# Kernel optimization log

Hardware: AMD Instinct MI355X
Metric: run time of the kernel (lower is better)

The kernel has to match this reference:

```python
import jax, jax.numpy as jnp
import numpy as np

E = 1024      # embed_dim
QH = 16       # query heads
KVH = 4       # kv heads
HD = E // QH  # head_dim = 64
KVE = HD * KVH  # 256
EPS = 1e-5
ROPE_BASE = 10000.0


def rope(x, d):
    # Faithful to the source RoPE: d == number of heads (x.shape[-2]),
    # and the 'sequence' axis of the cache is x.shape[0] (the batch dim).
    # rope(x) = x*cos + (x*sin) * neg_half(x)  (note: nonlinear in x).
    b = x.shape[0]
    theta = 1.0 / (ROPE_BASE ** (jnp.arange(0, d, 2, dtype=jnp.float32) / d))  # (d//2,)
    seq_idx = jnp.arange(b, dtype=jnp.float32)                                 # (b,)
    idx_theta = seq_idx[:, None] * theta[None, :]                              # (b, d//2)
    idx2 = jnp.concatenate([idx_theta, idx_theta], axis=-1)                    # (b, d)
    # cached shape (b,1,1,d); source permutes (0,1,3,2) -> (b,1,d,1)
    cos = jnp.cos(idx2)[:, None, :, None]  # (b,1,d,1)
    sin = jnp.sin(idx2)[:, None, :, None]
    d2 = d // 2
    # split of the LAST dim (head_dim) at d//2 == num_heads//2, as in source
    neg = jnp.concatenate([-x[..., d2:], x[..., :d2]], axis=-1)
    return x * cos + (x * sin) * neg


def setup_inputs() -> dict:
    key = jax.random.key(0)
    ks = jax.random.split(key, 12)
    b, n = 1, 2048

    def xavier(k, shape):
        fan_out, fan_in = shape
        std = (2.0 / (fan_in + fan_out)) ** 0.5
        return jax.random.normal(k, shape, dtype=jnp.float32) * std

    return {
        "query": jax.random.normal(ks[0], (b, n, E), dtype=jnp.float32),
        "key": jax.random.normal(ks[1], (b, n, E), dtype=jnp.float32),
        "value": jax.random.normal(ks[2], (b, n, E), dtype=jnp.float32),
        "Wq": xavier(ks[3], (E, E)),
        "bq": jnp.zeros((E,), jnp.float32),
        "Wk": xavier(ks[4], (KVE, E)),
        "bk": jnp.zeros((KVE,), jnp.float32),
        "Wv": xavier(ks[5], (KVE, E)),
        "bv": jnp.zeros((KVE,), jnp.float32),
        "gamma": jnp.ones((E,), jnp.float32),
        "beta": jnp.zeros((E,), jnp.float32),
    }


def reference(query, key, value, Wq, bq, Wk, bk, Wv, bv, gamma, beta):
    b, n, _ = query.shape
    q = query @ Wq.T + bq            # (b,n,E)
    k = key @ Wk.T + bk              # (b,n,KVE)
    v = value @ Wv.T + bv            # (b,n,KVE)

    q = q.reshape(b, n, QH, HD)      # b n h d
    k = k.reshape(b, n, KVH, HD)
    v = v.reshape(b, n, KVH, HD)

    q = rope(q, QH)
    k = rope(k, KVH)

    # b n h d -> b h n d
    q = jnp.transpose(q, (0, 2, 1, 3))
    k = jnp.transpose(k, (0, 2, 1, 3))
    v = jnp.transpose(v, (0, 2, 1, 3))

    scale = float(HD) ** 0.5
    q = q / scale

    g = QH // KVH
    # 'b (h g) n d -> b g h n d' : h outer, g inner
    q = q.reshape(b, KVH, g, n, HD)              # (b, h, g, n, d)
    q = jnp.transpose(q, (0, 2, 1, 3, 4))        # (b, g, h, n, d)

    sim = jnp.einsum('bghnd,bhsd->bghns', q, k)  # (b,g,h,n,s)
    attn = jax.nn.softmax(sim, axis=-1)
    out = jnp.einsum('bghns,bhsd->bghnd', attn, v)

    # 'b g h n d -> b n (h g) d'
    out = jnp.transpose(out, (0, 3, 2, 1, 4))    # (b, n, h, g, d)
    x = out.reshape(b, n, QH * HD)               # (b, n, E)

    # LayerNorm (biased variance, as in torch)
    mu = jnp.mean(x, axis=-1, keepdims=True)
    var = jnp.mean((x - mu) ** 2, axis=-1, keepdims=True)
    x = (x - mu) * jax.lax.rsqrt(var + EPS) * gamma + beta

    # NOTE: source computes out_proj(x) but returns x, so out_proj is dead code.
    return x
```

## Files before the change

kernel.cpp:

```cpp
#include <hip/hip_runtime.h>
#include <math.h>

#define EDIM   1024
#define KVEDIM 256
#define HDIM   64
#define QHEADS 16

typedef __attribute__((ext_vector_type(8))) short short8;
typedef __attribute__((ext_vector_type(4))) float f32x4;

__device__ __forceinline__ unsigned pack2(float a, float b) {
    unsigned ua = __builtin_bit_cast(unsigned, a);
    unsigned ub = __builtin_bit_cast(unsigned, b);
    ua += 0x7fffu + ((ua >> 16) & 1u);
    ub += 0x7fffu + ((ub >> 16) & 1u);
    return (ua >> 16) | (ub & 0xffff0000u);
}
__device__ __forceinline__ short f2b(float a) {
    unsigned ua = __builtin_bit_cast(unsigned, a);
    ua += 0x7fffu + ((ua >> 16) & 1u);
    return (short)(ua >> 16);
}
__device__ __forceinline__ unsigned cvtpk(float a, float b) {
    unsigned r;
    asm("v_cvt_pk_bf16_f32 %0, %1, %2" : "=v"(r) : "v"(a), "v"(b));
    return r;
}

__global__ __launch_bounds__(256)
void cvt_bf16(const float* __restrict__ s0, const float* __restrict__ s1,
              const float* __restrict__ s2, const float* __restrict__ s3,
              const float* __restrict__ s4, const float* __restrict__ s5,
              short* __restrict__ d0, short* __restrict__ d1,
              short* __restrict__ d2, short* __restrict__ d3,
              short* __restrict__ d4, short* __restrict__ d5,
              int n0, int n1, int n2, int n3, int n4, int n5)
{
    const float* s; short* d; int n;
    switch (blockIdx.y) {
        case 0: s = s0; d = d0; n = n0; break;
        case 1: s = s1; d = d1; n = n1; break;
        case 2: s = s2; d = d2; n = n2; break;
        case 3: s = s3; d = d3; n = n3; break;
        case 4: s = s4; d = d4; n = n4; break;
        default: s = s5; d = d5; n = n5; break;
    }
    int i = ((int)blockIdx.x * 256 + threadIdx.x) * 8;
    if (i >= n) return;
    float4 a = *(const float4*)&s[i];
    float4 b = *(const float4*)&s[i + 4];
    uint4 o;
    o.x = pack2(a.x, a.y); o.y = pack2(a.z, a.w);
    o.z = pack2(b.x, b.y); o.w = pack2(b.z, b.w);
    *(uint4*)&d[i] = o;
}

__global__ __launch_bounds__(256)
void proj_gemm(const short* __restrict__ Aq, const short* __restrict__ Ak,
               const short* __restrict__ Av,
               const short* __restrict__ Wqb, const short* __restrict__ Wkb,
               const short* __restrict__ Wvb,
               const float* __restrict__ bq, const float* __restrict__ bk,
               const float* __restrict__ bv,
               short* __restrict__ Cq, short* __restrict__ Ck,
               short* __restrict__ Cv, float qscale)
{
    const int bid = blockIdx.x;
    const short* A; const short* W; const float* bias; short* C;
    int N, bm, bn; float scale;
    if (bid < 128) {
        A = Aq; W = Wqb; bias = bq; C = Cq; N = EDIM; scale = qscale;
        bm = (bid >> 3) * 128; bn = (bid & 7) * 128;
    } else if (bid < 160) {
        int i = bid - 128;
        A = Ak; W = Wkb; bias = bk; C = Ck; N = KVEDIM; scale = 1.0f;
        bm = (i >> 1) * 128; bn = (i & 1) * 128;
    } else {
        int i = bid - 160;
        A = Av; W = Wvb; bias = bv; C = Cv; N = KVEDIM; scale = 1.0f;
        bm = (i >> 1) * 128; bn = (i & 1) * 128;
    }
    const int K = EDIM;

    __shared__ short As[128 * 72];
    __shared__ short Ws[128 * 72];

    const int t = threadIdx.x, lane = t & 63, wv = t >> 6;
    const int lm = lane & 15, quad = lane >> 4;
    const int q8 = quad * 8, q4 = quad * 4;
    const int wm = (wv & 1) * 64, wn = (wv >> 1) * 64;
    const int sr = t >> 3, sc = (t & 7) * 8;

    f32x4 zero = {0.f, 0.f, 0.f, 0.f};
    f32x4 acc[4][4];
    #pragma unroll
    for (int i = 0; i < 4; ++i)
        #pragma unroll
        for (int j = 0; j < 4; ++j) acc[i][j] = zero;

    for (int k0 = 0; k0 < K; k0 += 64) {
        __syncthreads();
        #pragma unroll
        for (int i = 0; i < 4; ++i) {
            int r = sr + i * 32;
            *(uint4*)&As[r * 72 + sc] = *(const uint4*)&A[(size_t)(bm + r) * K + k0 + sc];
            *(uint4*)&Ws[r * 72 + sc] = *(const uint4*)&W[(size_t)(bn + r) * K + k0 + sc];
        }
        __syncthreads();
        #pragma unroll
        for (int ks = 0; ks < 2; ++ks) {
            short8 af[4], bfr[4];
            #pragma unroll
            for (int i = 0; i < 4; ++i)
                af[i] = *(const short8*)&As[(wm + i * 16 + lm) * 72 + ks * 32 + q8];
            #pragma unroll
            for (int j = 0; j < 4; ++j)
                bfr[j] = *(const short8*)&Ws[(wn + j * 16 + lm) * 72 + ks * 32 + q8];
            #pragma unroll
            for (int i = 0; i < 4; ++i)
                #pragma unroll
                for (int j = 0; j < 4; ++j)
                    acc[i][j] = __builtin_amdgcn_mfma_f32_16x16x32_bf16(
                        af[i], bfr[j], acc[i][j], 0, 0, 0);
        }
    }

    #pragma unroll
    for (int j = 0; j < 4; ++j) {
        float bj = bias[bn + wn + j * 16 + lm];
        #pragma unroll
        for (int i = 0; i < 4; ++i)
            #pragma unroll
            for (int r = 0; r < 4; ++r)
                C[(size_t)(bm + wm + i * 16 + q4 + r) * N + bn + wn + j * 16 + lm] =
                    f2b((acc[i][j][r] + bj) * scale);
    }
}

__global__ __launch_bounds__(256, 4)
void attn_mfma(const short* __restrict__ q, const short* __restrict__ k,
               const short* __restrict__ v, float* __restrict__ x,
               float* __restrict__ opart, float* __restrict__ lpart,
               int n, int s_len, int partial)
{
    __shared__ short Ks[64 * 64];
    __shared__ short Vs[4096];

    const int kvh = blockIdx.y;
    const int r0  = blockIdx.x * 16;
    const int t = threadIdx.x, lane = t & 63, wv = t >> 6;
    const int qh = (kvh << 2) | wv;
    const int lm = lane & 15, quad = lane >> 4, q8 = quad * 8;

    short8 qf0, qf1;
    {
        const short* qp = &q[(size_t)(r0 + lm) * EDIM + qh * HDIM];
        qf0 = *(const short8*)&qp[q8];
        qf1 = *(const short8*)&qp[32 + q8];
    }

    const f32x4 zero = {0.f, 0.f, 0.f, 0.f};
    f32x4 oacc[4] = {zero, zero, zero, zero};
    float lp = 0.f;

    const int sr  = t >> 2;
    const int scs = (t & 3) * 16;
    const int kw0 = sr * 64 + (scs ^ ((sr & 7) << 3));
    const int kw1 = sr * 64 + ((scs + 8) ^ ((sr & 7) << 3));
    const int vs4 = (t & 15) * 4;
    const int vd0 = (t >> 4) * 4;
    const int vktp = vs4 >> 5, vqd = (vs4 >> 2) & 3, vhf = (vs4 >> 4) & 1;

    const int krx  = q8 ^ ((lm & 7) << 3);
    const int krx2 = (32 + q8) ^ ((lm & 7) << 3);

    const int s_lo = (int)blockIdx.z * s_len;
    const int s_hi = s_lo + s_len;
    const size_t kbase = (size_t)kvh * HDIM;

    uint4 kra, krb;
    uint2 vrr[4];
    {
        const uint4* ks = (const uint4*)&k[(size_t)(s_lo + sr) * KVEDIM + kbase + scs];
        kra = ks[0]; krb = ks[1];
        #pragma unroll
        for (int i = 0; i < 4; ++i)
            vrr[i] = *(const uint2*)&v[(size_t)(s_lo + vs4 + i) * KVEDIM + kbase + vd0];
    }

    for (int s0 = s_lo; s0 < s_hi; s0 += 64) {
        *(uint4*)&Ks[kw0] = kra;
        *(uint4*)&Ks[kw1] = krb;
        #pragma unroll
        for (int j = 0; j < 4; ++j) {
            const unsigned sel = (j & 1) ? 0x07060302u : 0x05040100u;
            unsigned a0 = (j < 2) ? vrr[0].x : vrr[0].y;
            unsigned a1 = (j < 2) ? vrr[1].x : vrr[1].y;
            unsigned a2 = (j < 2) ? vrr[2].x : vrr[2].y;
            unsigned a3 = (j < 2) ? vrr[3].x : vrr[3].y;
            uint2 o;
            o.x = __builtin_amdgcn_perm(a1, a0, sel);
            o.y = __builtin_amdgcn_perm(a3, a2, sel);
            const int dd = vd0 + j;
            int slot = ((dd >> 4) << 7) + (vktp << 6) + (vqd << 4) + (dd & 15);
            slot ^= (slot >> 4) & 7;
            *(uint2*)&Vs[slot * 8 + vhf * 4] = o;
        }
        __syncthreads();

        if (s0 + 64 < s_hi) {
            const uint4* ks = (const uint4*)&k[(size_t)(s0 + 64 + sr) * KVEDIM + kbase + scs];
            kra = ks[0]; krb = ks[1];
            #pragma unroll
            for (int i = 0; i < 4; ++i)
                vrr[i] = *(const uint2*)&v[(size_t)(s0 + 64 + vs4 + i) * KVEDIM + kbase + vd0];
        }

        uint2 pa[4];
        #pragma unroll
        for (int kt = 0; kt < 4; ++kt) {
            const int krow = (kt * 16 + lm) * 64;
            short8 kf0 = *(const short8*)&Ks[krow + krx];
            short8 kf1 = *(const short8*)&Ks[krow + krx2];
            f32x4 s = zero;
            s = __builtin_amdgcn_mfma_f32_16x16x32_bf16(kf0, qf0, s, 0, 0, 0);
            s = __builtin_amdgcn_mfma_f32_16x16x32_bf16(kf1, qf1, s, 0, 0, 0);
            float p0 = exp2f(s[0]), p1 = exp2f(s[1]);
            float p2 = exp2f(s[2]), p3 = exp2f(s[3]);
            lp += (p0 + p1) + (p2 + p3);
            pa[kt].x = cvtpk(p0, p1);
            pa[kt].y = cvtpk(p2, p3);
        }

        uint4 ap0; ap0.x = pa[0].x; ap0.y = pa[0].y; ap0.z = pa[1].x; ap0.w = pa[1].y;
        uint4 ap1; ap1.x = pa[2].x; ap1.y = pa[2].y; ap1.z = pa[3].x; ap1.w = pa[3].y;
        #pragma unroll
        for (int dt = 0; dt < 4; ++dt) {
            int sb  = (dt << 7) + (quad << 4) + lm;
            int sx0 = sb ^ ((sb >> 4) & 7);
            int sb1 = sb + 64;
            int sx1 = sb1 ^ ((sb1 >> 4) & 7);
            oacc[dt] = __builtin_amdgcn_mfma_f32_16x16x32_bf16(
                __builtin_bit_cast(short8, ap0),
                *(const short8*)&Vs[sx0 * 8], oacc[dt], 0, 0, 0);
            oacc[dt] = __builtin_amdgcn_mfma_f32_16x16x32_bf16(
                __builtin_bit_cast(short8, ap1),
                *(const short8*)&Vs[sx1 * 8], oacc[dt], 0, 0, 0);
        }
        __syncthreads();
    }

    float lt = lp;
    lt += __shfl_xor(lt, 16);
    lt += __shfl_xor(lt, 32);

    if (partial) {
        float* xp = opart + (size_t)blockIdx.z * n * EDIM;
        if (lane < 16)
            lpart[(size_t)blockIdx.z * n * QHEADS + (size_t)(r0 + lane) * QHEADS + qh] = lt;
        #pragma unroll
        for (int r = 0; r < 4; ++r) {
            const int row = r0 + quad * 4 + r;
            #pragma unroll
            for (int dt = 0; dt < 4; ++dt)
                xp[(size_t)row * EDIM + qh * HDIM + dt * 16 + lm] = oacc[dt][r];
        }
    } else {
        float linv[4];
        #pragma unroll
        for (int r = 0; r < 4; ++r)
            linv[r] = 1.0f / __shfl(lt, quad * 4 + r);
        #pragma unroll
        for (int r = 0; r < 4; ++r) {
            const int row = r0 + quad * 4 + r;
            #pragma unroll
            for (int dt = 0; dt < 4; ++dt)
                x[(size_t)row * EDIM + qh * HDIM + dt * 16 + lm] = oacc[dt][r] * linv[r];
        }
    }
}

__global__ __launch_bounds__(256)
void ln_kernel(float* __restrict__ x, const float* __restrict__ gamma,
               const float* __restrict__ beta,
               const float* __restrict__ opart, const float* __restrict__ lpart,
               int nsplit, int n)
{
    const int row = blockIdx.x;
    const int t = threadIdx.x;

    float4 xv;
    if (nsplit > 0) {
        const int head = t >> 4;
        float l = 0.f;
        float4 s = {0.f, 0.f, 0.f, 0.f};
        for (int z = 0; z < nsplit; ++z) {
            const float4 o = *(const float4*)&opart[(size_t)z * n * EDIM +
                                                    (size_t)row * EDIM + t * 4];
            s.x += o.x; s.y += o.y; s.z += o.z; s.w += o.w;
            l += lpart[(size_t)z * n * QHEADS + (size_t)row * QHEADS + head];
        }
        const float inv = 1.f / l;
        xv.x = s.x * inv; xv.y = s.y * inv; xv.z = s.z * inv; xv.w = s.w * inv;
    } else {
        xv = *(const float4*)&x[(size_t)row * EDIM + t * 4];
    }

    float sm  = xv.x + xv.y + xv.z + xv.w;
    float sq = xv.x * xv.x + xv.y * xv.y + xv.z * xv.z + xv.w * xv.w;
    #pragma unroll
    for (int m = 1; m < 64; m <<= 1) {
        sm += __shfl_xor(sm, m);
        sq += __shfl_xor(sq, m);
    }
    __shared__ float ws_[4], wq_[4];
    const int wave = t >> 6;
    if ((t & 63) == 0) { ws_[wave] = sm; wq_[wave] = sq; }
    __syncthreads();
    sm = ws_[0] + ws_[1] + ws_[2] + ws_[3];
    sq = wq_[0] + wq_[1] + wq_[2] + wq_[3];

    const float mu   = sm * (1.f / EDIM);
    const float var  = sq * (1.f / EDIM) - mu * mu;
    const float rstd = rsqrtf(var + 1e-5f);

    float4 g = *(const float4*)&gamma[t * 4];
    float4 b = *(const float4*)&beta[t * 4];
    float4 o;
    o.x = (xv.x - mu) * rstd * g.x + b.x;
    o.y = (xv.y - mu) * rstd * g.y + b.y;
    o.z = (xv.z - mu) * rstd * g.z + b.z;
    o.w = (xv.w - mu) * rstd * g.w + b.w;
    *(float4*)&x[(size_t)row * EDIM + t * 4] = o;
}

extern "C" void kernel_launch(void* const* d_in, const int* in_sizes, int n_in,
                              void* d_out, int out_size, void* d_ws, size_t ws_size,
                              hipStream_t stream)
{
    const float* query = (const float*)d_in[0];
    const float* key   = (const float*)d_in[1];
    const float* value = (const float*)d_in[2];
    const float* Wq    = (const float*)d_in[3];
    const float* bq    = (const float*)d_in[4];
    const float* Wk    = (const float*)d_in[5];
    const float* bk    = (const float*)d_in[6];
    const float* Wv    = (const float*)d_in[7];
    const float* bv    = (const float*)d_in[8];
    const float* gamma = (const float*)d_in[9];
    const float* beta  = (const float*)d_in[10];
    float* out = (float*)d_out;

    const int n = in_sizes[0] / EDIM;

    short* qa  = (short*)d_ws;
    short* ka  = qa  + (size_t)n * EDIM;
    short* va  = ka  + (size_t)n * EDIM;
    short* wqb = va  + (size_t)n * EDIM;
    short* wkb = wqb + (size_t)EDIM * EDIM;
    short* wvb = wkb + (size_t)KVEDIM * EDIM;
    short* qb  = wvb + (size_t)KVEDIM * EDIM;
    short* kb  = qb  + (size_t)n * EDIM;
    short* vb  = kb  + (size_t)n * KVEDIM;
    short* ws_end = vb + (size_t)n * KVEDIM;

    const size_t base_bytes = (size_t)((char*)ws_end - (char*)d_ws);
    int nsplit = 0;
    {
        const int cand = 2;
        size_t need = base_bytes +
                      (size_t)cand * ((size_t)n * EDIM + (size_t)n * QHEADS) * sizeof(float);
        if ((n % (64 * cand)) == 0 && need <= ws_size) nsplit = cand;
    }
    float* opart = (float*)ws_end;
    float* lpart = opart + (size_t)(nsplit > 0 ? nsplit : 1) * n * EDIM;

    const float qscale = 0.125f * 1.44269504088896f;

    cvt_bf16<<<dim3(1024, 6), 256, 0, stream>>>(
        query, key, value, Wq, Wk, Wv,
        qa, ka, va, wqb, wkb, wvb,
        n * EDIM, n * EDIM, n * EDIM, EDIM * EDIM, KVEDIM * EDIM, KVEDIM * EDIM);

    proj_gemm<<<dim3(192), 256, 0, stream>>>(
        qa, ka, va, wqb, wkb, wvb, bq, bk, bv, qb, kb, vb, qscale);

    const int zdim  = (nsplit > 0) ? nsplit : 1;
    const int s_len = n / zdim;
    attn_mfma<<<dim3(n / 16, 4, zdim), 256, 0, stream>>>(
        qb, kb, vb, out, opart, lpart, n, s_len, nsplit > 0 ? 1 : 0);

    ln_kernel<<<dim3(n), 256, 0, stream>>>(out, gamma, beta, opart, lpart, nsplit, n);
}
```

Before: 162.4 us.

## Fuse bf16 conversion into projection GEMM and double-buffer attention K/V tiles

Drops the standalone fp32-to-bf16 conversion kernel. The projection GEMM now loads fp32 inputs and weights directly and converts them with v_cvt_pk_bf16_f32 while filling shared memory, using 64x64 tiles so the grid has 768 blocks instead of 192. The attention kernel double-buffers its K/V shared tiles, which removes one barrier per iteration, and raises wave priority around the MFMA sections. The cost is that each GEMM block now reads fp32 data, so global traffic per tile doubles and A/W rows are converted redundantly across blocks. The smaller tiles also lower per-block data reuse.

```diff
diff --git a/kernel.cpp b/kernel.cpp
--- a/kernel.cpp
+++ b/kernel.cpp
@@ -9,13 +9,6 @@
 typedef __attribute__((ext_vector_type(8))) short short8;
 typedef __attribute__((ext_vector_type(4))) float f32x4;
 
-__device__ __forceinline__ unsigned pack2(float a, float b) {
-    unsigned ua = __builtin_bit_cast(unsigned, a);
-    unsigned ub = __builtin_bit_cast(unsigned, b);
-    ua += 0x7fffu + ((ua >> 16) & 1u);
-    ub += 0x7fffu + ((ub >> 16) & 1u);
-    return (ua >> 16) | (ub & 0xffff0000u);
-}
 __device__ __forceinline__ short f2b(float a) {
     unsigned ua = __builtin_bit_cast(unsigned, a);
     ua += 0x7fffu + ((ua >> 16) & 1u);
@@ -28,108 +21,90 @@
 }
 
 __global__ __launch_bounds__(256)
-void cvt_bf16(const float* __restrict__ s0, const float* __restrict__ s1,
-              const float* __restrict__ s2, const float* __restrict__ s3,
-              const float* __restrict__ s4, const float* __restrict__ s5,
-              short* __restrict__ d0, short* __restrict__ d1,
-              short* __restrict__ d2, short* __restrict__ d3,
-              short* __restrict__ d4, short* __restrict__ d5,
-              int n0, int n1, int n2, int n3, int n4, int n5)
-{
-    const float* s; short* d; int n;
-    switch (blockIdx.y) {
-        case 0: s = s0; d = d0; n = n0; break;
-        case 1: s = s1; d = d1; n = n1; break;
-        case 2: s = s2; d = d2; n = n2; break;
-        case 3: s = s3; d = d3; n = n3; break;
-        case 4: s = s4; d = d4; n = n4; break;
-        default: s = s5; d = d5; n = n5; break;
-    }
-    int i = ((int)blockIdx.x * 256 + threadIdx.x) * 8;
-    if (i >= n) return;
-    float4 a = *(const float4*)&s[i];
-    float4 b = *(const float4*)&s[i + 4];
-    uint4 o;
-    o.x = pack2(a.x, a.y); o.y = pack2(a.z, a.w);
-    o.z = pack2(b.x, b.y); o.w = pack2(b.z, b.w);
-    *(uint4*)&d[i] = o;
-}
-
-__global__ __launch_bounds__(256)
-void proj_gemm(const short* __restrict__ Aq, const short* __restrict__ Ak,
-               const short* __restrict__ Av,
-               const short* __restrict__ Wqb, const short* __restrict__ Wkb,
-               const short* __restrict__ Wvb,
+void proj_gemm(const float* __restrict__ Aq, const float* __restrict__ Ak,
+               const float* __restrict__ Av,
+               const float* __restrict__ Wqf, const float* __restrict__ Wkf,
+               const float* __restrict__ Wvf,
                const float* __restrict__ bq, const float* __restrict__ bk,
                const float* __restrict__ bv,
                short* __restrict__ Cq, short* __restrict__ Ck,
                short* __restrict__ Cv, float qscale)
 {
     const int bid = blockIdx.x;
-    const short* A; const short* W; const float* bias; short* C;
+    const float* A; const float* W; const float* bias; short* C;
     int N, bm, bn; float scale;
-    if (bid < 128) {
-        A = Aq; W = Wqb; bias = bq; C = Cq; N = EDIM; scale = qscale;
-        bm = (bid >> 3) * 128; bn = (bid & 7) * 128;
-    } else if (bid < 160) {
-        int i = bid - 128;
-        A = Ak; W = Wkb; bias = bk; C = Ck; N = KVEDIM; scale = 1.0f;
-        bm = (i >> 1) * 128; bn = (i & 1) * 128;
+    if (bid < 512) {
+        A = Aq; W = Wqf; bias = bq; C = Cq; N = EDIM; scale = qscale;
+        bm = (bid >> 4) * 64; bn = (bid & 15) * 64;
+    } else if (bid < 640) {
+        int i = bid - 512;
+        A = Ak; W = Wkf; bias = bk; C = Ck; N = KVEDIM; scale = 1.0f;
+        bm = (i >> 2) * 64; bn = (i & 3) * 64;
     } else {
-        int i = bid - 160;
-        A = Av; W = Wvb; bias = bv; C = Cv; N = KVEDIM; scale = 1.0f;
-        bm = (i >> 1) * 128; bn = (i & 1) * 128;
+        int i = bid - 640;
+        A = Av; W = Wvf; bias = bv; C = Cv; N = KVEDIM; scale = 1.0f;
+        bm = (i >> 2) * 64; bn = (i & 3) * 64;
     }
     const int K = EDIM;
 
-    __shared__ short As[128 * 72];
-    __shared__ short Ws[128 * 72];
+    __shared__ short As[64 * 72];
+    __shared__ short Ws[64 * 72];
 
     const int t = threadIdx.x, lane = t & 63, wv = t >> 6;
     const int lm = lane & 15, quad = lane >> 4;
     const int q8 = quad * 8, q4 = quad * 4;
-    const int wm = (wv & 1) * 64, wn = (wv >> 1) * 64;
-    const int sr = t >> 3, sc = (t & 7) * 8;
-
-    f32x4 zero = {0.f, 0.f, 0.f, 0.f};
-    f32x4 acc[4][4];
-    #pragma unroll
-    for (int i = 0; i < 4; ++i)
-        #pragma unroll
-        for (int j = 0; j < 4; ++j) acc[i][j] = zero;
+    const int wm = (wv & 1) * 32, wn = (wv >> 1) * 32;
+    const int sr = t >> 2, c0 = (t & 3) * 16;
+
+    const f32x4 zero = {0.f, 0.f, 0.f, 0.f};
+    f32x4 acc[2][2] = {{zero, zero}, {zero, zero}};
 
     for (int k0 = 0; k0 < K; k0 += 64) {
         __syncthreads();
-        #pragma unroll
-        for (int i = 0; i < 4; ++i) {
-            int r = sr + i * 32;
-            *(uint4*)&As[r * 72 + sc] = *(const uint4*)&A[(size_t)(bm + r) * K + k0 + sc];
-            *(uint4*)&Ws[r * 72 + sc] = *(const uint4*)&W[(size_t)(bn + r) * K + k0 + sc];
+        {
+            const float4* ap = (const float4*)&A[(size_t)(bm + sr) * K + k0 + c0];
+            float4 a0 = ap[0], a1 = ap[1], a2 = ap[2], a3 = ap[3];
+            uint4 o0, o1;
+            o0.x = cvtpk(a0.x, a0.y); o0.y = cvtpk(a0.z, a0.w);
+            o0.z = cvtpk(a1.x, a1.y); o0.w = cvtpk(a1.z, a1.w);
+            o1.x = cvtpk(a2.x, a2.y); o1.y = cvtpk(a2.z, a2.w);
+            o1.z = cvtpk(a3.x, a3.y); o1.w = cvtpk(a3.z, a3.w);
+            *(uint4*)&As[sr * 72 + c0]     = o0;
+            *(uint4*)&As[sr * 72 + c0 + 8] = o1;
+            const float4* wp = (const float4*)&W[(size_t)(bn + sr) * K + k0 + c0];
+            float4 w0 = wp[0], w1 = wp[1], w2 = wp[2], w3 = wp[3];
+            uint4 p0, p1;
+            p0.x = cvtpk(w0.x, w0.y); p0.y = cvtpk(w0.z, w0.w);
+            p0.z = cvtpk(w1.x, w1.y); p0.w = cvtpk(w1.z, w1.w);
+            p1.x = cvtpk(w2.x, w2.y); p1.y = cvtpk(w2.z, w2.w);
+            p1.z = cvtpk(w3.x, w3.y); p1.w = cvtpk(w3.z, w3.w);
+            *(uint4*)&Ws[sr * 72 + c0]     = p0;
+            *(uint4*)&Ws[sr * 72 + c0 + 8] = p1;
         }
         __syncthreads();
         #pragma unroll
         for (int ks = 0; ks < 2; ++ks) {
-            short8 af[4], bfr[4];
-            #pragma unroll
-            for (int i = 0; i < 4; ++i)
+            short8 af[2], bfr[2];
+            #pragma unroll
+            for (int i = 0; i < 2; ++i)
                 af[i] = *(const short8*)&As[(wm + i * 16 + lm) * 72 + ks * 32 + q8];
             #pragma unroll
-            for (int j = 0; j < 4; ++j)
+            for (int j = 0; j < 2; ++j)
                 bfr[j] = *(const short8*)&Ws[(wn + j * 16 + lm) * 72 + ks * 32 + q8];
             #pragma unroll
-            for (int i = 0; i < 4; ++i)
+            for (int i = 0; i < 2; ++i)
                 #pragma unroll
-                for (int j = 0; j < 4; ++j)
+                for (int j = 0; j < 2; ++j)
                     acc[i][j] = __builtin_amdgcn_mfma_f32_16x16x32_bf16(
                         af[i], bfr[j], acc[i][j], 0, 0, 0);
         }
     }
 
     #pragma unroll
-    for (int j = 0; j < 4; ++j) {
+    for (int j = 0; j < 2; ++j) {
         float bj = bias[bn + wn + j * 16 + lm];
         #pragma unroll
-        for (int i = 0; i < 4; ++i)
+        for (int i = 0; i < 2; ++i)
             #pragma unroll
             for (int r = 0; r < 4; ++r)
                 C[(size_t)(bm + wm + i * 16 + q4 + r) * N + bn + wn + j * 16 + lm] =
@@ -143,8 +118,8 @@
                float* __restrict__ opart, float* __restrict__ lpart,
                int n, int s_len, int partial)
 {
-    __shared__ short Ks[64 * 64];
-    __shared__ short Vs[4096];
+    __shared__ short Ks[2][64 * 64];
+    __shared__ short Vs[2][4096];
 
     const int kvh = blockIdx.y;
     const int r0  = blockIdx.x * 16;
@@ -175,11 +150,12 @@
     const int krx2 = (32 + q8) ^ ((lm & 7) << 3);
 
     const int s_lo = (int)blockIdx.z * s_len;
-    const int s_hi = s_lo + s_len;
+    const int nt = s_len >> 6;
     const size_t kbase = (size_t)kvh * HDIM;
 
     uint4 kra, krb;
     uint2 vrr[4];
+
     {
         const uint4* ks = (const uint4*)&k[(size_t)(s_lo + sr) * KVEDIM + kbase + scs];
         kra = ks[0]; krb = ks[1];
@@ -187,10 +163,9 @@
         for (int i = 0; i < 4; ++i)
             vrr[i] = *(const uint2*)&v[(size_t)(s_lo + vs4 + i) * KVEDIM + kbase + vd0];
     }
-
-    for (int s0 = s_lo; s0 < s_hi; s0 += 64) {
-        *(uint4*)&Ks[kw0] = kra;
-        *(uint4*)&Ks[kw1] = krb;
+    {
+        *(uint4*)&Ks[0][kw0] = kra;
+        *(uint4*)&Ks[0][kw1] = krb;
         #pragma unroll
         for (int j = 0; j < 4; ++j) {
             const unsigned sel = (j & 1) ? 0x07060302u : 0x05040100u;
@@ -204,27 +179,34 @@
             const int dd = vd0 + j;
             int slot = ((dd >> 4) << 7) + (vktp << 6) + (vqd << 4) + (dd & 15);
             slot ^= (slot >> 4) & 7;
-            *(uint2*)&Vs[slot * 8 + vhf * 4] = o;
-        }
+            *(uint2*)&Vs[0][slot * 8 + vhf * 4] = o;
+        }
+    }
+
+    int cur = 0;
+    for (int it = 0; it < nt; ++it) {
+        if (it + 1 < nt) {
+            const int s1 = s_lo + (it + 1) * 64;
+            const uint4* ks = (const uint4*)&k[(size_t)(s1 + sr) * KVEDIM + kbase + scs];
+            kra = ks[0]; krb = ks[1];
+            #pragma unroll
+            for (int i = 0; i < 4; ++i)
+                vrr[i] = *(const uint2*)&v[(size_t)(s1 + vs4 + i) * KVEDIM + kbase + vd0];
+        }
+
         __syncthreads();
-
-        if (s0 + 64 < s_hi) {
-            const uint4* ks = (const uint4*)&k[(size_t)(s0 + 64 + sr) * KVEDIM + kbase + scs];
-            kra = ks[0]; krb = ks[1];
-            #pragma unroll
-            for (int i = 0; i < 4; ++i)
-                vrr[i] = *(const uint2*)&v[(size_t)(s0 + 64 + vs4 + i) * KVEDIM + kbase + vd0];
-        }
 
         uint2 pa[4];
         #pragma unroll
         for (int kt = 0; kt < 4; ++kt) {
             const int krow = (kt * 16 + lm) * 64;
-            short8 kf0 = *(const short8*)&Ks[krow + krx];
-            short8 kf1 = *(const short8*)&Ks[krow + krx2];
+            short8 kf0 = *(const short8*)&Ks[cur][krow + krx];
+            short8 kf1 = *(const short8*)&Ks[cur][krow + krx2];
             f32x4 s = zero;
+            __builtin_amdgcn_s_setprio(1);
             s = __builtin_amdgcn_mfma_f32_16x16x32_bf16(kf0, qf0, s, 0, 0, 0);
             s = __builtin_amdgcn_mfma_f32_16x16x32_bf16(kf1, qf1, s, 0, 0, 0);
+            __builtin_amdgcn_s_setprio(0);
             float p0 = exp2f(s[0]), p1 = exp2f(s[1]);
             float p2 = exp2f(s[2]), p3 = exp2f(s[3]);
             lp += (p0 + p1) + (p2 + p3);
@@ -234,6 +216,7 @@
 
         uint4 ap0; ap0.x = pa[0].x; ap0.y = pa[0].y; ap0.z = pa[1].x; ap0.w = pa[1].y;
         uint4 ap1; ap1.x = pa[2].x; ap1.y = pa[2].y; ap1.z = pa[3].x; ap1.w = pa[3].y;
+        __builtin_amdgcn_s_setprio(1);
         #pragma unroll
         for (int dt = 0; dt < 4; ++dt) {
             int sb  = (dt << 7) + (quad << 4) + lm;
@@ -242,12 +225,34 @@
             int sx1 = sb1 ^ ((sb1 >> 4) & 7);
             oacc[dt] = __builtin_amdgcn_mfma_f32_16x16x32_bf16(
                 __builtin_bit_cast(short8, ap0),
-                *(const short8*)&Vs[sx0 * 8], oacc[dt], 0, 0, 0);
+                *(const short8*)&Vs[cur][sx0 * 8], oacc[dt], 0, 0, 0);
             oacc[dt] = __builtin_amdgcn_mfma_f32_16x16x32_bf16(
                 __builtin_bit_cast(short8, ap1),
-                *(const short8*)&Vs[sx1 * 8], oacc[dt], 0, 0, 0);
-        }
-        __syncthreads();
+                *(const short8*)&Vs[cur][sx1 * 8], oacc[dt], 0, 0, 0);
+        }
+        __builtin_amdgcn_s_setprio(0);
+
+        if (it + 1 < nt) {
+            const int nxt = cur ^ 1;
+            *(uint4*)&Ks[nxt][kw0] = kra;
+            *(uint4*)&Ks[nxt][kw1] = krb;
+            #pragma unroll
+            for (int j = 0; j < 4; ++j) {
+                const unsigned sel = (j & 1) ? 0x07060302u : 0x05040100u;
+                unsigned a0 = (j < 2) ? vrr[0].x : vrr[0].y;
+                unsigned a1 = (j < 2) ? vrr[1].x : vrr[1].y;
+                unsigned a2 = (j < 2) ? vrr[2].x : vrr[2].y;
+                unsigned a3 = (j < 2) ? vrr[3].x : vrr[3].y;
+                uint2 o;
+                o.x = __builtin_amdgcn_perm(a1, a0, sel);
+                o.y = __builtin_amdgcn_perm(a3, a2, sel);
+                const int dd = vd0 + j;
+                int slot = ((dd >> 4) << 7) + (vktp << 6) + (vqd << 4) + (dd & 15);
+                slot ^= (slot >> 4) & 7;
+                *(uint2*)&Vs[nxt][slot * 8 + vhf * 4] = o;
+            }
+        }
+        cur ^= 1;
     }
 
     float lt = lp;
@@ -353,15 +358,9 @@
 
     const int n = in_sizes[0] / EDIM;
 
-    short* qa  = (short*)d_ws;
-    short* ka  = qa  + (size_t)n * EDIM;
-    short* va  = ka  + (size_t)n * EDIM;
-    short* wqb = va  + (size_t)n * EDIM;
-    short* wkb = wqb + (size_t)EDIM * EDIM;
-    short* wvb = wkb + (size_t)KVEDIM * EDIM;
-    short* qb  = wvb + (size_t)KVEDIM * EDIM;
-    short* kb  = qb  + (size_t)n * EDIM;
-    short* vb  = kb  + (size_t)n * KVEDIM;
+    short* qb  = (short*)d_ws;
+    short* kb  = qb + (size_t)n * EDIM;
+    short* vb  = kb + (size_t)n * KVEDIM;
     short* ws_end = vb + (size_t)n * KVEDIM;
 
     const size_t base_bytes = (size_t)((char*)ws_end - (char*)d_ws);
@@ -377,13 +376,8 @@
 
     const float qscale = 0.125f * 1.44269504088896f;
 
-    cvt_bf16<<<dim3(1024, 6), 256, 0, stream>>>(
-        query, key, value, Wq, Wk, Wv,
-        qa, ka, va, wqb, wkb, wvb,
-        n * EDIM, n * EDIM, n * EDIM, EDIM * EDIM, KVEDIM * EDIM, KVEDIM * EDIM);
-
-    proj_gemm<<<dim3(192), 256, 0, stream>>>(
-        qa, ka, va, wqb, wkb, wvb, bq, bk, bv, qb, kb, vb, qscale);
+    proj_gemm<<<dim3(768), 256, 0, stream>>>(
+        query, key, value, Wq, Wk, Wv, bq, bk, bv, qb, kb, vb, qscale);
 
     const int zdim  = (nsplit > 0) ? nsplit : 1;
     const int s_len = n / zdim;
```

Measured after the change: 165.5 us. Within noise of the previous version (+1.9%).
